# Kernel tuning notes

Measured on AMD Instinct MI355X. Metric: run time of the kernel, lower is better.

Reference implementation:

```python
import jax, jax.numpy as jnp
import numpy as np

B, S, D, H = 2, 2048, 1024, 16
DK = D // H

def setup_inputs() -> dict:
    key = jax.random.key(0)
    ks = jax.random.split(key, 12)
    scale = 1.0 / np.sqrt(D)
    return {
        "q": jax.random.normal(ks[0], (B, S, D), jnp.float32),
        "k": jax.random.normal(ks[1], (B, S, D), jnp.float32),
        "v": jax.random.normal(ks[2], (B, S, D), jnp.float32),
        "mask": jax.random.randint(ks[3], (B, 1, S, S), 0, 2, jnp.int32),
        "w_q": jax.random.normal(ks[4], (D, D), jnp.float32) * scale,
        "b_q": jnp.zeros((D,), jnp.float32),
        "w_k": jax.random.normal(ks[5], (D, D), jnp.float32) * scale,
        "b_k": jnp.zeros((D,), jnp.float32),
        "w_v": jax.random.normal(ks[6], (D, D), jnp.float32) * scale,
        "b_v": jnp.zeros((D,), jnp.float32),
        "w_o": jax.random.normal(ks[7], (D, D), jnp.float32) * scale,
        "b_o": jnp.zeros((D,), jnp.float32),
    }

def reference(q, k, v, mask, w_q, b_q, w_k, b_k, w_v, b_v, w_o, b_o):
    # projections (nn.Linear: x @ W^T + b)
    Q = q @ w_q.T + b_q  # [B,S,D]
    K = k @ w_k.T + b_k
    V = v @ w_v.T + b_v
    # split heads -> [B,H,S,DK]
    Q = Q.reshape(B, S, H, DK).transpose(0, 2, 1, 3)
    K = K.reshape(B, S, H, DK).transpose(0, 2, 1, 3)
    V = V.reshape(B, S, H, DK).transpose(0, 2, 1, 3)
    scores = jnp.einsum("bhqd,bhkd->bhqk", Q, K) / jnp.sqrt(jnp.float32(DK))
    scores = jnp.where(mask == 0, jnp.float32(-1e9), scores)
    attn = jax.nn.softmax(scores, axis=-1)  # dropout p=0 -> identity
    x = jnp.einsum("bhqk,bhkd->bhqd", attn, V)
    x = x.transpose(0, 2, 1, 3).reshape(B, S, D)
    return x @ w_o.T + b_o
```

## Files before the change

kernel.cpp:

```cpp
#include <hip/hip_runtime.h>
#include <hip/hip_bf16.h>
#include <cstdint>
#include <cstddef>

typedef short bf16x8 __attribute__((ext_vector_type(8)));
typedef short bf16x4v __attribute__((ext_vector_type(4)));
typedef float f32x4 __attribute__((ext_vector_type(4)));
typedef unsigned int uint32x2 __attribute__((ext_vector_type(2)));
typedef __hip_bfloat16 bf16;

constexpr int Bb = 2, Ss = 2048, Dd = 1024, Hh = 16, DKk = 64;

__device__ __forceinline__ void async_lds16(void* lds, const void* g) {
  __builtin_amdgcn_global_load_lds(
      (const __attribute__((address_space(1))) void*)g,
      (__attribute__((address_space(3))) void*)lds, 16, 0, 0);
}

__device__ __forceinline__ float bf2f(bf16 x) { return __bfloat162float(x); }
__device__ __forceinline__ short f2bf(float x) {
  bf16 h = __float2bfloat16(x);
  return *(short*)&h;
}
__device__ __forceinline__ short f2bf_fast(float x) {
  return (short)((__float_as_uint(x) + 0x8000u) >> 16);
}
__device__ __forceinline__ float bfs2f(short s) {
  return __uint_as_float(((uint32_t)(uint16_t)s) << 16);
}
__device__ __forceinline__ uint32_t cvtpk_bf16(float lo, float hi) {
  uint32_t r;
  asm("v_cvt_pk_bf16_f32 %0, %1, %2" : "=v"(r) : "v"(lo), "v"(hi));
  return r;
}
__device__ __forceinline__ uint32x2 pl32swap(uint32_t d, uint32_t s) {
  return __builtin_amdgcn_permlane32_swap(d, s, false, false);
}
__device__ __forceinline__ uint32x2 pl16swap(uint32_t d, uint32_t s) {
  return __builtin_amdgcn_permlane16_swap(d, s, false, false);
}

struct CvtArgs {
  const float* src[12];
  short* dst[12];
  int n[12];
  int count;
};

__global__ __launch_bounds__(256)
void cvt_all(CvtArgs a, const int* __restrict__ mask, uint32_t* __restrict__ bits)
{
  const int t = blockIdx.y;
  if (t == 11) {
    const int stride = 1024 * 256;
    int i = blockIdx.x * 256 + threadIdx.x;
#pragma unroll 4
    for (int it = 0; it < 32; ++it, i += stride) {
      const unsigned long long bal = __ballot(mask[i] != 0);
      if ((threadIdx.x & 63) == 0)
        *(unsigned long long*)(bits + (i >> 5)) = bal;
    }
    return;
  }
  if (t >= a.count) return;
  const float* s = a.src[t];
  short* d = a.dst[t];
  const int n = a.n[t];
  const int stride = gridDim.x * blockDim.x * 4;
  for (int i = (blockIdx.x * blockDim.x + threadIdx.x) * 4; i < n; i += stride) {
    const float4 v = *(const float4*)(s + i);
    bf16x4v o;
    o[0] = f2bf(v.x); o[1] = f2bf(v.y); o[2] = f2bf(v.z); o[3] = f2bf(v.w);
    *(bf16x4v*)(d + i) = o;
  }
}

__global__ __launch_bounds__(256, 3)
void gemm_bt(const bf16* __restrict__ A0, const bf16* __restrict__ A1, const bf16* __restrict__ A2,
             const bf16* __restrict__ W0, const bf16* __restrict__ W1, const bf16* __restrict__ W2,
             const bf16* __restrict__ b0, const bf16* __restrict__ b1, const bf16* __restrict__ b2,
             void* __restrict__ O0, void* __restrict__ O1, void* __restrict__ O2,
             float scale0, int vtrans)
{
  extern __shared__ char smem[];
  const int mt  = blockIdx.x;
  const int by  = blockIdx.y;
  const int mat = by >> 3;
  const int nt  = by & 7;
  const bf16* A    = (mat == 0) ? A0 : (mat == 1) ? A1 : A2;
  const bf16* W    = (mat == 0) ? W0 : (mat == 1) ? W1 : W2;
  const bf16* bias = (mat == 0) ? b0 : (mat == 1) ? b1 : b2;
  void*       Out  = (mat == 0) ? O0 : (mat == 1) ? O1 : O2;
  const float scale = (mat == 0) ? scale0 : 1.0f;

  const int tid  = threadIdx.x;
  const int w    = tid >> 6;
  const int lane = tid & 63;
  const int quad = lane >> 4;
  const int l16  = lane & 15;
  const int wm   = (w & 1) * 64;
  const int wn   = (w >> 1) * 64;

  const int srow = lane >> 3;
  const int sseg = (lane & 7) ^ srow;

  const char* Abytes = (const char*)A;
  const char* Wbytes = (const char*)W;

  f32x4 acc[4][4];
#pragma unroll
  for (int i = 0; i < 4; ++i)
#pragma unroll
    for (int j = 0; j < 4; ++j) acc[i][j] = f32x4{0.f, 0.f, 0.f, 0.f};

  for (int kt = 0; kt < 16; ++kt) {
    __syncthreads();
#pragma unroll
    for (int c = 0; c < 4; ++c) {
      const int r0 = w * 32 + c * 8;
      async_lds16(smem + r0 * 128,
                  Abytes + (size_t)(mt * 128 + r0 + srow) * 2048 + kt * 128 + sseg * 16);
      async_lds16(smem + 16384 + r0 * 128,
                  Wbytes + (size_t)(nt * 128 + r0 + srow) * 2048 + kt * 128 + sseg * 16);
    }
    __syncthreads();
#pragma unroll
    for (int s = 0; s < 2; ++s) {
      bf16x8 af[4], bfg[4];
#pragma unroll
      for (int mb = 0; mb < 4; ++mb) {
        const int row = wm + mb * 16 + l16;
        af[mb] = *(const bf16x8*)(smem + row * 128 + (((4 * s + quad) ^ (row & 7)) * 16));
      }
#pragma unroll
      for (int nb = 0; nb < 4; ++nb) {
        const int row = wn + nb * 16 + l16;
        bfg[nb] = *(const bf16x8*)(smem + 16384 + row * 128 + (((4 * s + quad) ^ (row & 7)) * 16));
      }
#pragma unroll
      for (int mb = 0; mb < 4; ++mb)
#pragma unroll
        for (int nb = 0; nb < 4; ++nb)
          acc[mb][nb] = __builtin_amdgcn_mfma_f32_16x16x32_bf16(af[mb], bfg[nb], acc[mb][nb], 0, 0, 0);
    }
  }

  if (vtrans && mat == 2) {
    __syncthreads();
#pragma unroll
    for (int nb = 0; nb < 4; ++nb) {
      const int dk = wn + nb * 16 + l16;
      const float bv = bf2f(bias[nt * 128 + dk]);
#pragma unroll
      for (int mb = 0; mb < 4; ++mb) {
        const int s0 = wm + mb * 16 + quad * 4;
        bf16x4v pk;
#pragma unroll
        for (int r = 0; r < 4; ++r) pk[r] = f2bf_fast(acc[mb][nb][r] + bv);
        *(bf16x4v*)(smem + dk * 256 + (((s0 >> 3) ^ (dk & 15)) * 16) + (s0 & 7) * 2) = pk;
      }
    }
    __syncthreads();
    const int bidx  = (mt * 128) >> 11;
    const int sbase = (mt * 128) & 2047;
#pragma unroll
    for (int i = 0; i < 8; ++i) {
      const int dk  = i * 16 + (tid >> 4);
      const int seg = tid & 15;
      bf16x8 vrow = *(const bf16x8*)(smem + dk * 256 + ((seg ^ (dk & 15)) * 16));
      *(bf16x8*)((bf16*)Out + (size_t)bidx * 2097152 + (size_t)(nt * 128 + dk) * 2048
                 + sbase + seg * 8) = vrow;
    }
  } else {
#pragma unroll
    for (int nb = 0; nb < 4; ++nb) {
      const int col = nt * 128 + wn + nb * 16 + l16;
      const float bv = bf2f(bias[col]);
#pragma unroll
      for (int mb = 0; mb < 4; ++mb) {
#pragma unroll
        for (int r = 0; r < 4; ++r) {
          const int row = mt * 128 + wm + mb * 16 + quad * 4 + r;
          short s = f2bf_fast((acc[mb][nb][r] + bv) * scale);
          ((short*)Out)[(size_t)row * 1024 + col] = s;
        }
      }
    }
  }
}

__global__ __launch_bounds__(256, 4)
void gemm_out(const bf16* __restrict__ A, const bf16* __restrict__ W,
              const bf16* __restrict__ bias, float* __restrict__ Out)
{
  __shared__ char smem[16384];
  const int mt = blockIdx.x;
  const int nt = blockIdx.y;
  const int tid = threadIdx.x, w = tid >> 6, lane = tid & 63;
  const int quad = lane >> 4, l16 = lane & 15;
  const int wm = (w & 1) * 32, wn = (w >> 1) * 32;
  const int srow = lane >> 3;
  const int sseg = (lane & 7) ^ (srow & 7);

  const char* Abytes = (const char*)A;
  const char* Wbytes = (const char*)W;

  f32x4 acc[2][2];
#pragma unroll
  for (int i = 0; i < 2; ++i)
#pragma unroll
    for (int j = 0; j < 2; ++j) acc[i][j] = f32x4{0.f, 0.f, 0.f, 0.f};

  for (int kt = 0; kt < 16; ++kt) {
    __syncthreads();
#pragma unroll
    for (int c = 0; c < 2; ++c) {
      const int r0 = c * 32 + w * 8;
      async_lds16(smem + c * 4096 + w * 1024,
                  Abytes + (size_t)(mt * 64 + r0 + srow) * 2048 + kt * 128 + sseg * 16);
      async_lds16(smem + 8192 + c * 4096 + w * 1024,
                  Wbytes + (size_t)(nt * 64 + r0 + srow) * 2048 + kt * 128 + sseg * 16);
    }
    __syncthreads();
#pragma unroll
    for (int s = 0; s < 2; ++s) {
      bf16x8 af[2], bfg[2];
#pragma unroll
      for (int mb = 0; mb < 2; ++mb) {
        const int row = wm + mb * 16 + l16;
        af[mb] = *(const bf16x8*)(smem + row * 128 + (((4 * s + quad) ^ (row & 7)) * 16));
      }
#pragma unroll
      for (int nb = 0; nb < 2; ++nb) {
        const int row = wn + nb * 16 + l16;
        bfg[nb] = *(const bf16x8*)(smem + 8192 + row * 128 + (((4 * s + quad) ^ (row & 7)) * 16));
      }
#pragma unroll
      for (int mb = 0; mb < 2; ++mb)
#pragma unroll
        for (int nb = 0; nb < 2; ++nb)
          acc[mb][nb] = __builtin_amdgcn_mfma_f32_16x16x32_bf16(af[mb], bfg[nb], acc[mb][nb], 0, 0, 0);
    }
  }

#pragma unroll
  for (int nb = 0; nb < 2; ++nb) {
    const int col = nt * 64 + wn + nb * 16 + l16;
    const float bv = bf2f(bias[col]);
#pragma unroll
    for (int mb = 0; mb < 2; ++mb) {
#pragma unroll
      for (int r = 0; r < 4; ++r) {
        const int row = mt * 64 + wm + mb * 16 + quad * 4 + r;
        Out[(size_t)row * 1024 + col] = acc[mb][nb][r] + bv;
      }
    }
  }
}

__global__ __launch_bounds__(256, 4)
void attn(const bf16* __restrict__ Qp, const bf16* __restrict__ Kp,
          const bf16* __restrict__ VpT, const uint32_t* __restrict__ mbits,
          bf16* __restrict__ Opart, float* __restrict__ Lpart)
{
  __shared__ char smem[32768];
  char* Kb = smem;
  char* Vt = smem + 16384;

  const int tile  = blockIdx.x;
  const int split = blockIdx.y;
  const int qt = tile & 15, h = (tile >> 4) & 15, b = tile >> 8;
  const int tid = threadIdx.x, w = tid >> 6, lane = tid & 63;
  const int quad = lane >> 4, l16 = lane & 15;
  const int qb = qt * 128;
  const size_t headoff = (size_t)b * (Ss * Dd) + h * DKk;

  const int kc0 = (split == 0) ? 0 : (split == 1) ? 6 : 11;
  const int kc1 = (split == 0) ? 6 : (split == 1) ? 11 : 16;

  bf16x8 qf[2][2];
#pragma unroll
  for (int set = 0; set < 2; ++set)
#pragma unroll
    for (int s2 = 0; s2 < 2; ++s2) {
      const int row = qb + w * 32 + set * 16 + l16;
      qf[set][s2] = *(const bf16x8*)(Qp + headoff + (size_t)row * Dd + s2 * 32 + quad * 8);
    }

  f32x4 o[2][4];
  float Lacc[2] = {0.f, 0.f};
#pragma unroll
  for (int set = 0; set < 2; ++set)
#pragma unroll
    for (int nbk = 0; nbk < 4; ++nbk) o[set][nbk] = f32x4{0.f, 0.f, 0.f, 0.f};

  const uint32_t* mrow0 = mbits + (size_t)(b * Ss + qb + w * 32 + l16) * 64;
  const uint32_t* mrow1 = mrow0 + 16 * 64;

  for (int kc = kc0; kc < kc1; ++kc) {
    const int kb = kc * 128;
    __syncthreads();
#pragma unroll
    for (int c = 0; c < 4; ++c) {
      {
        const int row = c * 32 + w * 8 + (lane >> 3);
        const int seg = (lane & 7) ^ (row & 7);
        async_lds16(Kb + c * 4096 + w * 1024,
                    Kp + headoff + (size_t)(kb + row) * Dd + seg * 8);
      }
      {
        const int row = c * 16 + w * 4 + (lane >> 4);
        const int seg = (lane & 15) ^ (row & 15);
        async_lds16(Vt + c * 4096 + w * 1024,
                    VpT + (size_t)b * 2097152 + (size_t)(h * 64 + row) * 2048 + kb + seg * 8);
      }
    }
    __syncthreads();

    const uint4 mwv0 = *(const uint4*)(mrow0 + kc * 4);
    const uint4 mwv1 = *(const uint4*)(mrow1 + kc * 4);
    const uint32_t mw0[4] = {mwv0.x, mwv0.y, mwv0.z, mwv0.w};
    const uint32_t mw1[4] = {mwv1.x, mwv1.y, mwv1.z, mwv1.w};

#pragma unroll
    for (int sl = 0; sl < 4; ++sl) {
      f32x4 sc[2][2];
#pragma unroll
      for (int set = 0; set < 2; ++set)
#pragma unroll
        for (int nbh = 0; nbh < 2; ++nbh) sc[set][nbh] = f32x4{0.f, 0.f, 0.f, 0.f};
#pragma unroll
      for (int s2 = 0; s2 < 2; ++s2)
#pragma unroll
        for (int nbh = 0; nbh < 2; ++nbh) {
          const int row = (sl * 2 + nbh) * 16 + l16;
          bf16x8 kf = *(const bf16x8*)(Kb + row * 128 + (((s2 * 4 + quad) ^ (row & 7)) * 16));
          sc[0][nbh] = __builtin_amdgcn_mfma_f32_16x16x32_bf16(kf, qf[0][s2], sc[0][nbh], 0, 0, 0);
          sc[1][nbh] = __builtin_amdgcn_mfma_f32_16x16x32_bf16(kf, qf[1][s2], sc[1][nbh], 0, 0, 0);
        }

      bf16x8 pf[2];
#pragma unroll
      for (int set = 0; set < 2; ++set) {
        const uint32_t mword = (set == 0) ? mw0[sl] : mw1[sl];
        uint32_t pk[2][2];
        float Ls = 0.f;
#pragma unroll
        for (int nbh = 0; nbh < 2; ++nbh) {
          const uint32_t nib = (mword >> (nbh * 16 + quad * 4)) & 0xFu;
          const float e0 = __builtin_amdgcn_exp2f(sc[set][nbh][0]);
          const float e1 = __builtin_amdgcn_exp2f(sc[set][nbh][1]);
          const float e2 = __builtin_amdgcn_exp2f(sc[set][nbh][2]);
          const float e3 = __builtin_amdgcn_exp2f(sc[set][nbh][3]);
          const float p0 = (nib & 1u) ? e0 : 0.f;
          const float p1 = (nib & 2u) ? e1 : 0.f;
          const float p2 = (nib & 4u) ? e2 : 0.f;
          const float p3 = (nib & 8u) ? e3 : 0.f;
          Ls += (p0 + p1) + (p2 + p3);
          pk[nbh][0] = cvtpk_bf16(p0, p1);
          pk[nbh][1] = cvtpk_bf16(p2, p3);
        }
        Lacc[set] += Ls;
        const uint32x2 r0 = pl32swap(pk[0][0], pk[1][0]);
        const uint32x2 r1 = pl32swap(pk[0][1], pk[1][1]);
        const uint32x2 t0 = pl16swap(r0.x, r0.y);
        const uint32x2 t1 = pl16swap(r1.x, r1.y);
        union { uint32_t u[4]; bf16x8 v; } U;
        U.u[0] = t0.x; U.u[1] = t1.x; U.u[2] = t0.y; U.u[3] = t1.y;
        pf[set] = U.v;
      }

#pragma unroll
      for (int nbk = 0; nbk < 4; ++nbk) {
        const int row = nbk * 16 + l16;
        bf16x8 vf = *(const bf16x8*)(Vt + row * 256 + (((sl * 4 + quad) ^ (row & 15)) * 16));
        o[0][nbk] = __builtin_amdgcn_mfma_f32_16x16x32_bf16(pf[0], vf, o[0][nbk], 0, 0, 0);
        o[1][nbk] = __builtin_amdgcn_mfma_f32_16x16x32_bf16(pf[1], vf, o[1][nbk], 0, 0, 0);
      }
    }
  }

#pragma unroll
  for (int set = 0; set < 2; ++set) {
    float Lq = Lacc[set];
    Lq += __shfl_xor(Lq, 16);
    Lq += __shfl_xor(Lq, 32);
    const int rbase = tile * 128 + w * 32 + set * 16;
#pragma unroll
    for (int r = 0; r < 4; ++r) {
      const int rglob = rbase + quad * 4 + r;
#pragma unroll
      for (int nbk = 0; nbk < 4; ++nbk) {
        short s = f2bf_fast(o[set][nbk][r]);
        ((short*)Opart)[((size_t)split * 65536 + rglob) * 64 + nbk * 16 + l16] = s;
      }
    }
    if (quad == 0)
      Lpart[(size_t)split * 65536 + rbase + l16] = Lq;
  }
}

__global__ __launch_bounds__(256)
void combine(const bf16* __restrict__ Opart, const float* __restrict__ Lpart,
             bf16* __restrict__ Xa)
{
  const int t = threadIdx.x;
  const int row = blockIdx.x * 32 + (t >> 3);
  const int dkc = (t & 7) * 8;
  const float L = Lpart[row] + Lpart[65536 + row] + Lpart[131072 + row];
  const float inv = 1.0f / L;
  const bf16x8 O0 = *(const bf16x8*)(Opart + (size_t)row * 64 + dkc);
  const bf16x8 O1 = *(const bf16x8*)(Opart + ((size_t)65536 + row) * 64 + dkc);
  const bf16x8 O2 = *(const bf16x8*)(Opart + ((size_t)131072 + row) * 64 + dkc);
  bf16x8 res;
#pragma unroll
  for (int j = 0; j < 8; ++j)
    res[j] = f2bf_fast((bfs2f(O0[j]) + bfs2f(O1[j]) + bfs2f(O2[j])) * inv);
  const int tile = row >> 7, qlocal = row & 127;
  const int b = tile >> 8, h = (tile >> 4) & 15, q = (tile & 15) * 128 + qlocal;
  *(bf16x8*)(Xa + (size_t)(b * 2048 + q) * 1024 + h * 64 + dkc) = res;
}

extern "C" void kernel_launch(void* const* d_in, const int* in_sizes, int n_in,
                              void* d_out, int out_size, void* d_ws, size_t ws_size,
                              hipStream_t stream)
{
  const float* q  = (const float*)d_in[0];
  const float* k  = (const float*)d_in[1];
  const float* v  = (const float*)d_in[2];
  const int*   mk = (const int*)d_in[3];
  const float* wq = (const float*)d_in[4];
  const float* bq = (const float*)d_in[5];
  const float* wk = (const float*)d_in[6];
  const float* bk = (const float*)d_in[7];
  const float* wv = (const float*)d_in[8];
  const float* bv = (const float*)d_in[9];
  const float* wo = (const float*)d_in[10];
  const float* bo = (const float*)d_in[11];
  float* out = (float*)d_out;

  char* ws = (char*)d_ws;
  bf16* qb_  = (bf16*)(ws + ((size_t)0  << 20));
  bf16* kb_  = (bf16*)(ws + ((size_t)8  << 20));
  bf16* vb_  = (bf16*)(ws + ((size_t)16 << 20));
  bf16* Qp   = (bf16*)(ws + ((size_t)24 << 20));
  bf16* Kp   = (bf16*)(ws + ((size_t)32 << 20));
  bf16* VpT  = (bf16*)(ws + ((size_t)40 << 20));
  bf16* wqb  = (bf16*)(ws + ((size_t)48 << 20));
  bf16* wkb  = (bf16*)(ws + ((size_t)50 << 20));
  bf16* wvb  = (bf16*)(ws + ((size_t)52 << 20));
  bf16* wob  = (bf16*)(ws + ((size_t)54 << 20));
  bf16* bqb  = (bf16*)(ws + ((size_t)56 << 20));
  bf16* bkb  = (bf16*)(ws + ((size_t)56 << 20) + 2048);
  bf16* bvb  = (bf16*)(ws + ((size_t)56 << 20) + 4096);
  bf16* bob  = (bf16*)(ws + ((size_t)56 << 20) + 6144);
  uint32_t* mbits = (uint32_t*)(ws + ((size_t)56 << 20) + 65536);
  bf16*  Opart = (bf16*)(ws + ((size_t)0 << 20));
  float* Lpart = (float*)(ws + ((size_t)48 << 20));
  bf16*  Xa    = (bf16*)(ws + ((size_t)24 << 20));

  const int NA = Bb * Ss * Dd;
  const int NW = Dd * Dd;

  CvtArgs ca;
  ca.src[0] = q;  ca.dst[0] = (short*)qb_; ca.n[0] = NA;
  ca.src[1] = k;  ca.dst[1] = (short*)kb_; ca.n[1] = NA;
  ca.src[2] = v;  ca.dst[2] = (short*)vb_; ca.n[2] = NA;
  ca.src[3] = wq; ca.dst[3] = (short*)wqb; ca.n[3] = NW;
  ca.src[4] = wk; ca.dst[4] = (short*)wkb; ca.n[4] = NW;
  ca.src[5] = wv; ca.dst[5] = (short*)wvb; ca.n[5] = NW;
  ca.src[6] = wo; ca.dst[6] = (short*)wob; ca.n[6] = NW;
  ca.src[7] = bq; ca.dst[7] = (short*)bqb; ca.n[7] = Dd;
  ca.src[8] = bk; ca.dst[8] = (short*)bkb; ca.n[8] = Dd;
  ca.src[9] = bv; ca.dst[9] = (short*)bvb; ca.n[9] = Dd;
  ca.src[10] = bo; ca.dst[10] = (short*)bob; ca.n[10] = Dd;
  ca.src[11] = bo; ca.dst[11] = (short*)bob; ca.n[11] = 0;
  ca.count = 11;

  dim3 blk(256);
  cvt_all<<<dim3(1024, 12), blk, 0, stream>>>(ca, mk, mbits);

  gemm_bt<<<dim3(32, 24), blk, 32768, stream>>>(qb_, kb_, vb_, wqb, wkb, wvb,
                                                bqb, bkb, bvb,
                                                (void*)Qp, (void*)Kp, (void*)VpT,
                                                0.125f * 1.44269504088896340736f, 1);
  attn<<<dim3(512, 3), blk, 0, stream>>>(Qp, Kp, VpT, mbits, Opart, Lpart);
  combine<<<dim3(2048), blk, 0, stream>>>(Opart, Lpart, Xa);
  gemm_out<<<dim3(64, 16), blk, 0, stream>>>(Xa, wob, bob, out);
}
```

Before: 264.4 us.

## Double-buffer K/V staging in attention, use 2-way split and MFMA row sums

```diff
diff --git a/kernel.cpp b/kernel.cpp
--- a/kernel.cpp
+++ b/kernel.cpp
@@ -258,14 +258,29 @@
   }
 }
 
-__global__ __launch_bounds__(256, 4)
+__device__ __forceinline__ void stage_kv(char* KbB, char* VtB,
+    const bf16* __restrict__ Kp, const bf16* __restrict__ VpT,
+    size_t headoff, size_t vbase, int kb, int w, int lane)
+{
+#pragma unroll
+  for (int c = 0; c < 4; ++c) {
+    const int rowK = c * 32 + w * 8 + (lane >> 3);
+    const int segK = (lane & 7) ^ (rowK & 7);
+    async_lds16(KbB + c * 4096 + w * 1024,
+                Kp + headoff + (size_t)(kb + rowK) * Dd + segK * 8);
+    const int rowV = c * 16 + w * 4 + (lane >> 4);
+    const int segV = (lane & 15) ^ (rowV & 15);
+    async_lds16(VtB + c * 4096 + w * 1024,
+                VpT + vbase + (size_t)rowV * 2048 + kb + segV * 8);
+  }
+}
+
+__global__ __launch_bounds__(256, 2)
 void attn(const bf16* __restrict__ Qp, const bf16* __restrict__ Kp,
           const bf16* __restrict__ VpT, const uint32_t* __restrict__ mbits,
           bf16* __restrict__ Opart, float* __restrict__ Lpart)
 {
-  __shared__ char smem[32768];
-  char* Kb = smem;
-  char* Vt = smem + 16384;
+  __shared__ char smem[65536];
 
   const int tile  = blockIdx.x;
   const int split = blockIdx.y;
@@ -274,9 +289,10 @@
   const int quad = lane >> 4, l16 = lane & 15;
   const int qb = qt * 128;
   const size_t headoff = (size_t)b * (Ss * Dd) + h * DKk;
-
-  const int kc0 = (split == 0) ? 0 : (split == 1) ? 6 : 11;
-  const int kc1 = (split == 0) ? 6 : (split == 1) ? 11 : 16;
+  const size_t vbase = (size_t)b * 2097152 + (size_t)h * 131072;
+
+  const int kc0 = split * 8;
+  const int kc1 = kc0 + 8;
 
   bf16x8 qf[2][2];
 #pragma unroll
@@ -287,40 +303,46 @@
       qf[set][s2] = *(const bf16x8*)(Qp + headoff + (size_t)row * Dd + s2 * 32 + quad * 8);
     }
 
+  bf16x8 onesv;
+#pragma unroll
+  for (int j = 0; j < 8; ++j) onesv[j] = (short)0x3F80;
+
   f32x4 o[2][4];
-  float Lacc[2] = {0.f, 0.f};
-#pragma unroll
-  for (int set = 0; set < 2; ++set)
+  f32x4 oL[2];
+#pragma unroll
+  for (int set = 0; set < 2; ++set) {
+    oL[set] = f32x4{0.f, 0.f, 0.f, 0.f};
 #pragma unroll
     for (int nbk = 0; nbk < 4; ++nbk) o[set][nbk] = f32x4{0.f, 0.f, 0.f, 0.f};
+  }
 
   const uint32_t* mrow0 = mbits + (size_t)(b * Ss + qb + w * 32 + l16) * 64;
   const uint32_t* mrow1 = mrow0 + 16 * 64;
 
+  char* KbC = smem;
+  char* VtC = smem + 16384;
+  char* KbN = smem + 32768;
+  char* VtN = smem + 49152;
+
+  uint4 mc0v = *(const uint4*)(mrow0 + kc0 * 4);
+  uint4 mc1v = *(const uint4*)(mrow1 + kc0 * 4);
+  stage_kv(KbC, VtC, Kp, VpT, headoff, vbase, kc0 * 128, w, lane);
+
   for (int kc = kc0; kc < kc1; ++kc) {
-    const int kb = kc * 128;
-    __syncthreads();
-#pragma unroll
-    for (int c = 0; c < 4; ++c) {
-      {
-        const int row = c * 32 + w * 8 + (lane >> 3);
-        const int seg = (lane & 7) ^ (row & 7);
-        async_lds16(Kb + c * 4096 + w * 1024,
-                    Kp + headoff + (size_t)(kb + row) * Dd + seg * 8);
-      }
-      {
-        const int row = c * 16 + w * 4 + (lane >> 4);
-        const int seg = (lane & 15) ^ (row & 15);
-        async_lds16(Vt + c * 4096 + w * 1024,
-                    VpT + (size_t)b * 2097152 + (size_t)(h * 64 + row) * 2048 + kb + seg * 8);
-      }
-    }
-    __syncthreads();
-
-    const uint4 mwv0 = *(const uint4*)(mrow0 + kc * 4);
-    const uint4 mwv1 = *(const uint4*)(mrow1 + kc * 4);
-    const uint32_t mw0[4] = {mwv0.x, mwv0.y, mwv0.z, mwv0.w};
-    const uint32_t mw1[4] = {mwv1.x, mwv1.y, mwv1.z, mwv1.w};
+    uint4 mn0v = mc0v, mn1v = mc1v;
+    if (kc + 1 < kc1) {
+      mn0v = *(const uint4*)(mrow0 + (kc + 1) * 4);
+      mn1v = *(const uint4*)(mrow1 + (kc + 1) * 4);
+      stage_kv(KbN, VtN, Kp, VpT, headoff, vbase, (kc + 1) * 128, w, lane);
+      asm volatile("s_waitcnt vmcnt(8)" ::: "memory");
+    } else {
+      asm volatile("s_waitcnt vmcnt(0)" ::: "memory");
+    }
+    __builtin_amdgcn_s_barrier();
+    __builtin_amdgcn_sched_barrier(0);
+
+    const uint32_t mc0a[4] = {mc0v.x, mc0v.y, mc0v.z, mc0v.w};
+    const uint32_t mc1a[4] = {mc1v.x, mc1v.y, mc1v.z, mc1v.w};
 
 #pragma unroll
     for (int sl = 0; sl < 4; ++sl) {
@@ -329,22 +351,23 @@
       for (int set = 0; set < 2; ++set)
 #pragma unroll
         for (int nbh = 0; nbh < 2; ++nbh) sc[set][nbh] = f32x4{0.f, 0.f, 0.f, 0.f};
+      __builtin_amdgcn_s_setprio(1);
 #pragma unroll
       for (int s2 = 0; s2 < 2; ++s2)
 #pragma unroll
         for (int nbh = 0; nbh < 2; ++nbh) {
           const int row = (sl * 2 + nbh) * 16 + l16;
-          bf16x8 kf = *(const bf16x8*)(Kb + row * 128 + (((s2 * 4 + quad) ^ (row & 7)) * 16));
+          bf16x8 kf = *(const bf16x8*)(KbC + row * 128 + (((s2 * 4 + quad) ^ (row & 7)) * 16));
           sc[0][nbh] = __builtin_amdgcn_mfma_f32_16x16x32_bf16(kf, qf[0][s2], sc[0][nbh], 0, 0, 0);
           sc[1][nbh] = __builtin_amdgcn_mfma_f32_16x16x32_bf16(kf, qf[1][s2], sc[1][nbh], 0, 0, 0);
         }
+      __builtin_amdgcn_s_setprio(0);
 
       bf16x8 pf[2];
 #pragma unroll
       for (int set = 0; set < 2; ++set) {
-        const uint32_t mword = (set == 0) ? mw0[sl] : mw1[sl];
+        const uint32_t mword = (set == 0) ? mc0a[sl] : mc1a[sl];
         uint32_t pk[2][2];
-        float Ls = 0.f;
 #pragma unroll
         for (int nbh = 0; nbh < 2; ++nbh) {
           const uint32_t nib = (mword >> (nbh * 16 + quad * 4)) & 0xFu;
@@ -356,11 +379,9 @@
           const float p1 = (nib & 2u) ? e1 : 0.f;
           const float p2 = (nib & 4u) ? e2 : 0.f;
           const float p3 = (nib & 8u) ? e3 : 0.f;
-          Ls += (p0 + p1) + (p2 + p3);
           pk[nbh][0] = cvtpk_bf16(p0, p1);
           pk[nbh][1] = cvtpk_bf16(p2, p3);
         }
-        Lacc[set] += Ls;
         const uint32x2 r0 = pl32swap(pk[0][0], pk[1][0]);
         const uint32x2 r1 = pl32swap(pk[0][1], pk[1][1]);
         const uint32x2 t0 = pl16swap(r0.x, r0.y);
@@ -370,21 +391,30 @@
         pf[set] = U.v;
       }
 
+      __builtin_amdgcn_s_setprio(1);
+      oL[0] = __builtin_amdgcn_mfma_f32_16x16x32_bf16(pf[0], onesv, oL[0], 0, 0, 0);
+      oL[1] = __builtin_amdgcn_mfma_f32_16x16x32_bf16(pf[1], onesv, oL[1], 0, 0, 0);
 #pragma unroll
       for (int nbk = 0; nbk < 4; ++nbk) {
         const int row = nbk * 16 + l16;
-        bf16x8 vf = *(const bf16x8*)(Vt + row * 256 + (((sl * 4 + quad) ^ (row & 15)) * 16));
+        bf16x8 vf = *(const bf16x8*)(VtC + row * 256 + (((sl * 4 + quad) ^ (row & 15)) * 16));
         o[0][nbk] = __builtin_amdgcn_mfma_f32_16x16x32_bf16(pf[0], vf, o[0][nbk], 0, 0, 0);
         o[1][nbk] = __builtin_amdgcn_mfma_f32_16x16x32_bf16(pf[1], vf, o[1][nbk], 0, 0, 0);
       }
-    }
+      __builtin_amdgcn_s_setprio(0);
+    }
+
+    asm volatile("" ::: "memory");
+    __builtin_amdgcn_s_barrier();
+
+    char* tp;
+    tp = KbC; KbC = KbN; KbN = tp;
+    tp = VtC; VtC = VtN; VtN = tp;
+    mc0v = mn0v; mc1v = mn1v;
   }
 
 #pragma unroll
   for (int set = 0; set < 2; ++set) {
-    float Lq = Lacc[set];
-    Lq += __shfl_xor(Lq, 16);
-    Lq += __shfl_xor(Lq, 32);
     const int rbase = tile * 128 + w * 32 + set * 16;
 #pragma unroll
     for (int r = 0; r < 4; ++r) {
@@ -395,8 +425,11 @@
         ((short*)Opart)[((size_t)split * 65536 + rglob) * 64 + nbk * 16 + l16] = s;
       }
     }
-    if (quad == 0)
-      Lpart[(size_t)split * 65536 + rbase + l16] = Lq;
+    if (l16 == 0) {
+#pragma unroll
+      for (int r = 0; r < 4; ++r)
+        Lpart[(size_t)split * 65536 + rbase + quad * 4 + r] = oL[set][r];
+    }
   }
 }
 
@@ -407,15 +440,14 @@
   const int t = threadIdx.x;
   const int row = blockIdx.x * 32 + (t >> 3);
   const int dkc = (t & 7) * 8;
-  const float L = Lpart[row] + Lpart[65536 + row] + Lpart[131072 + row];
+  const float L = Lpart[row] + Lpart[65536 + row];
   const float inv = 1.0f / L;
   const bf16x8 O0 = *(const bf16x8*)(Opart + (size_t)row * 64 + dkc);
   const bf16x8 O1 = *(const bf16x8*)(Opart + ((size_t)65536 + row) * 64 + dkc);
-  const bf16x8 O2 = *(const bf16x8*)(Opart + ((size_t)131072 + row) * 64 + dkc);
   bf16x8 res;
 #pragma unroll
   for (int j = 0; j < 8; ++j)
-    res[j] = f2bf_fast((bfs2f(O0[j]) + bfs2f(O1[j]) + bfs2f(O2[j])) * inv);
+    res[j] = f2bf_fast((bfs2f(O0[j]) + bfs2f(O1[j])) * inv);
   const int tile = row >> 7, qlocal = row & 127;
   const int b = tile >> 8, h = (tile >> 4) & 15, q = (tile & 15) * 128 + qlocal;
   *(bf16x8*)(Xa + (size_t)(b * 2048 + q) * 1024 + h * 64 + dkc) = res;
@@ -484,7 +516,7 @@
                                                 bqb, bkb, bvb,
                                                 (void*)Qp, (void*)Kp, (void*)VpT,
                                                 0.125f * 1.44269504088896340736f, 1);
-  attn<<<dim3(512, 3), blk, 0, stream>>>(Qp, Kp, VpT, mbits, Opart, Lpart);
+  attn<<<dim3(512, 2), blk, 0, stream>>>(Qp, Kp, VpT, mbits, Opart, Lpart);
   combine<<<dim3(2048), blk, 0, stream>>>(Opart, Lpart, Xa);
   gemm_out<<<dim3(64, 16), blk, 0, stream>>>(Xa, wob, bob, out);
 }
```

Measured after the change: 254.9 us. 3.6% less time.
